# Kernel tuning notes

Measured on AMD Instinct MI355X. Metric: run time of the kernel, lower is better.

## Reference

```python
import jax, jax.numpy as jnp
import numpy as np

# Production-scale detection head dims
B_TOTAL = 16      # num_tbins(4) * batch_size(4)
NUM_ANCHORS = 100000
NUM_CLASSES = 8


def setup_inputs() -> dict:
    key = jax.random.key(0)
    k1, k2, k3, k4 = jax.random.split(key, 4)
    # anchors [A,4] = (cx, cy, w, h); widths/heights strictly positive
    ctr = jax.random.uniform(k1, (NUM_ANCHORS, 2), jnp.float32) * 512.0
    wh = jax.random.uniform(k2, (NUM_ANCHORS, 2), jnp.float32) * 64.0 + 8.0
    anchors = jnp.concatenate([ctr, wh], axis=-1)
    loc_preds = jax.random.normal(k3, (B_TOTAL, NUM_ANCHORS, 4), jnp.float32)
    # class scores in [0,1] (post-sigmoid semantics)
    cls_preds = jax.nn.sigmoid(jax.random.normal(k4, (B_TOTAL, NUM_ANCHORS, NUM_CLASSES), jnp.float32))
    return {
        "anchors": anchors,
        "loc_preds": loc_preds,
        "cls_preds": cls_preds,
        "varx": 0.1,
        "vary": 0.2,
        "score_thresh": 0.7,
        "batch_size": 4,
    }


def reference(anchors, loc_preds, cls_preds, varx, vary, score_thresh, batch_size):
    """Anchor decode + score-threshold filtering.

    Faithful to BoxDecoder.forward, but jit-compatible: instead of
    boolean-mask compaction into ragged per-(t,i) lists (data-dependent
    shapes), we return the dense [B*A*C, 6] box tensor plus the keep mask
    and batch_index; (mask, batch_index) fully determine the ragged
    targets[t][i] = box_tensor[mask & (batch_index == t*batch_size+i)].
    """
    B, A, C = cls_preds.shape
    # decode: xy = loc[:2]*varx*anchor_wh + anchor_xy ; wh = exp(loc[2:]*vary)*anchor_wh
    xy = loc_preds[..., :2] * varx * anchors[..., 2:] + anchors[..., :2]
    wh = jnp.exp(loc_preds[..., 2:] * vary) * anchors[..., 2:]
    box_preds = jnp.concatenate([xy - wh * 0.5, xy + wh * 0.5], axis=-1)  # [B,A,4]
    # expand boxes over classes, flatten to [B*A*C, ...] (same order as torch view(-1,...))
    boxes = jnp.broadcast_to(box_preds[:, :, None, :], (B, A, C, 4)).reshape(-1, 4)
    scores = cls_preds.reshape(-1)
    # idxs = b*C + c  ->  label = c+1, batch_index = b
    labels = jnp.broadcast_to(jnp.arange(C, dtype=jnp.float32) + 1.0, (B, A, C)).reshape(-1)
    batch_index = jnp.broadcast_to(jnp.arange(B, dtype=jnp.int32)[:, None, None], (B, A, C)).reshape(-1)
    box_tensor = jnp.concatenate([boxes, scores[:, None], labels[:, None]], axis=1)  # [B*A*C, 6]
    mask = scores >= score_thresh  # keep mask (compaction left to consumer / kernel)
    return box_tensor, mask, batch_index
```

## Files before the change

### kernel.cpp

```cpp
#include <hip/hip_runtime.h>
#include <math.h>


#define MAGIC_SHIFT 38

__global__ __launch_bounds__(256) void box_decode_kernel(
    const float4* __restrict__ anchors,
    const float4* __restrict__ loc,
    const float*  __restrict__ cls,
    const float*  __restrict__ varx_p,
    const float*  __restrict__ vary_p,
    const float*  __restrict__ th_p,
    float4*       __restrict__ out_box4,
    float4*       __restrict__ out_mask4,
    float4*       __restrict__ out_bidx4,
    unsigned n4,
    unsigned nm4,
    unsigned nb_box,
    unsigned A, unsigned C,
    unsigned f4_per_t,
    unsigned long long invA,
    unsigned long long invC,
    unsigned long long invF)
{
    unsigned tid = threadIdx.x;

    if (blockIdx.x < nb_box) {
        unsigned g = blockIdx.x * 256u + tid;
        if (g >= n4) return;

        unsigned t  = (unsigned)(((unsigned long long)g * invF) >> MAGIC_SHIFT);
        unsigned j  = g - t * f4_per_t;
        unsigned b  = (unsigned)(((unsigned long long)t * invA) >> MAGIC_SHIFT);
        unsigned a  = t - b * A;
        unsigned s  = j / 3u;
        unsigned jm = j - s * 3u;

        float varx = *varx_p;
        float vary = *vary_p;

        float4 anc = anchors[a];
        float4 lp  = loc[t];

        float x = fmaf(lp.x * varx, anc.z, anc.x);
        float y = fmaf(lp.y * varx, anc.w, anc.y);
        float w = expf(lp.z * vary) * anc.z;
        float h = expf(lp.w * vary) * anc.w;

        float x1 = fmaf(w, -0.5f, x);
        float y1 = fmaf(h, -0.5f, y);
        float x2 = fmaf(w,  0.5f, x);
        float y2 = fmaf(h,  0.5f, y);

        unsigned r0 = t * C + 2u * s;

        float4 r;
        if (jm == 0u) {
            r.x = x1; r.y = y1; r.z = x2; r.w = y2;
        } else if (jm == 1u) {
            r.x = cls[r0];
            r.y = (float)(2u * s + 1u);
            r.z = x1; r.w = y1;
        } else {
            r.x = x2; r.y = y2;
            r.z = cls[r0 + 1u];
            r.w = (float)(2u * s + 2u);
        }
        out_box4[g] = r;
    } else {
        unsigned k = (blockIdx.x - nb_box) * 256u + tid;
        if (k >= nm4) return;

        float th = *th_p;
        const float4* cls4 = (const float4*)cls;
        float4 sc = cls4[k];

        unsigned row0 = k * 4u;
        unsigned t2 = (unsigned)(((unsigned long long)row0 * invC) >> MAGIC_SHIFT);
        unsigned b  = (unsigned)(((unsigned long long)t2  * invA) >> MAGIC_SHIFT);
        float bf = (float)b;

        float4 m;
        m.x = (sc.x >= th) ? 1.0f : 0.0f;
        m.y = (sc.y >= th) ? 1.0f : 0.0f;
        m.z = (sc.z >= th) ? 1.0f : 0.0f;
        m.w = (sc.w >= th) ? 1.0f : 0.0f;
        out_mask4[k] = m;

        float4 bv; bv.x = bf; bv.y = bf; bv.z = bf; bv.w = bf;
        out_bidx4[k] = bv;
    }
}

extern "C" void kernel_launch(void* const* d_in, const int* in_sizes, int n_in,
                              void* d_out, int out_size, void* d_ws, size_t ws_size,
                              hipStream_t stream) {
    const float* anchors = (const float*)d_in[0];
    const float* loc     = (const float*)d_in[1];
    const float* cls     = (const float*)d_in[2];
    const float* varx_p  = (const float*)d_in[3];
    const float* vary_p  = (const float*)d_in[4];
    const float* th_p    = (const float*)d_in[5];

    unsigned A = (unsigned)(in_sizes[0] / 4);
    unsigned B = (unsigned)((unsigned)in_sizes[1] / (4u * A));
    unsigned C = (unsigned)((unsigned)in_sizes[2] / (A * B));
    unsigned rows = B * A * C;

    unsigned f4_per_t = (6u * C) / 4u;
    unsigned n4  = rows * 6u / 4u;
    unsigned nm4 = rows / 4u;

    float* out_box  = (float*)d_out;
    float* out_mask = out_box + (size_t)rows * 6;
    float* out_bidx = out_mask + rows;

    unsigned long long invA = ((1ULL << MAGIC_SHIFT) / A) + 1ULL;
    unsigned long long invC = ((1ULL << MAGIC_SHIFT) / C) + 1ULL;
    unsigned long long invF = ((1ULL << MAGIC_SHIFT) / f4_per_t) + 1ULL;

    unsigned nb_box  = (n4  + 255u) / 256u;
    unsigned nb_mask = (nm4 + 255u) / 256u;

    box_decode_kernel<<<dim3(nb_box + nb_mask), dim3(256), 0, stream>>>(
        (const float4*)anchors, (const float4*)loc, cls,
        varx_p, vary_p, th_p,
        (float4*)out_box, (float4*)out_mask, (float4*)out_bidx,
        n4, nm4, nb_box, A, C, f4_per_t, invA, invC, invF);
}
```

Before: 523.2 us.

## Fuse mask and batch-index writes into box threads with nontemporal stores

Removes the separate mask/batch-index block range. The box threads that already read each score now also write that score's mask and batch index as scalar stores, so cls is read once. All output stores become nontemporal to avoid polluting cache on this write-heavy stream. The tradeoff is that the mask and bidx writes change from float4 to scattered scalar stores, two thirds of threads now write extra, and the box threads become more divergent.

```diff
diff --git a/kernel.cpp b/kernel.cpp
--- a/kernel.cpp
+++ b/kernel.cpp
@@ -3,6 +3,8 @@
 
 
 #define MAGIC_SHIFT 38
+
+typedef float vfloat4 __attribute__((ext_vector_type(4)));
 
 __global__ __launch_bounds__(256) void box_decode_kernel(
     const float4* __restrict__ anchors,
@@ -11,85 +13,64 @@
     const float*  __restrict__ varx_p,
     const float*  __restrict__ vary_p,
     const float*  __restrict__ th_p,
-    float4*       __restrict__ out_box4,
-    float4*       __restrict__ out_mask4,
-    float4*       __restrict__ out_bidx4,
+    vfloat4*      __restrict__ out_box4,
+    float*        __restrict__ out_mask,
+    float*        __restrict__ out_bidx,
     unsigned n4,
-    unsigned nm4,
-    unsigned nb_box,
     unsigned A, unsigned C,
     unsigned f4_per_t,
     unsigned long long invA,
-    unsigned long long invC,
     unsigned long long invF)
 {
-    unsigned tid = threadIdx.x;
+    unsigned g = blockIdx.x * 256u + threadIdx.x;
+    if (g >= n4) return;
 
-    if (blockIdx.x < nb_box) {
-        unsigned g = blockIdx.x * 256u + tid;
-        if (g >= n4) return;
+    unsigned t  = (unsigned)(((unsigned long long)g * invF) >> MAGIC_SHIFT);
+    unsigned j  = g - t * f4_per_t;
+    unsigned b  = (unsigned)(((unsigned long long)t * invA) >> MAGIC_SHIFT);
+    unsigned a  = t - b * A;
+    unsigned s  = j / 3u;
+    unsigned jm = j - s * 3u;
 
-        unsigned t  = (unsigned)(((unsigned long long)g * invF) >> MAGIC_SHIFT);
-        unsigned j  = g - t * f4_per_t;
-        unsigned b  = (unsigned)(((unsigned long long)t * invA) >> MAGIC_SHIFT);
-        unsigned a  = t - b * A;
-        unsigned s  = j / 3u;
-        unsigned jm = j - s * 3u;
+    float varx = *varx_p;
+    float vary = *vary_p;
+    float th   = *th_p;
 
-        float varx = *varx_p;
-        float vary = *vary_p;
+    float4 anc = anchors[a];
+    float4 lp  = loc[t];
 
-        float4 anc = anchors[a];
-        float4 lp  = loc[t];
+    float x = fmaf(lp.x * varx, anc.z, anc.x);
+    float y = fmaf(lp.y * varx, anc.w, anc.y);
+    float w = expf(lp.z * vary) * anc.z;
+    float h = expf(lp.w * vary) * anc.w;
 
-        float x = fmaf(lp.x * varx, anc.z, anc.x);
-        float y = fmaf(lp.y * varx, anc.w, anc.y);
-        float w = expf(lp.z * vary) * anc.z;
-        float h = expf(lp.w * vary) * anc.w;
+    float x1 = fmaf(w, -0.5f, x);
+    float y1 = fmaf(h, -0.5f, y);
+    float x2 = fmaf(w,  0.5f, x);
+    float y2 = fmaf(h,  0.5f, y);
 
-        float x1 = fmaf(w, -0.5f, x);
-        float y1 = fmaf(h, -0.5f, y);
-        float x2 = fmaf(w,  0.5f, x);
-        float y2 = fmaf(h,  0.5f, y);
+    unsigned r0 = t * C + 2u * s;
+    float bf = (float)b;
 
-        unsigned r0 = t * C + 2u * s;
-
-        float4 r;
-        if (jm == 0u) {
-            r.x = x1; r.y = y1; r.z = x2; r.w = y2;
-        } else if (jm == 1u) {
-            r.x = cls[r0];
-            r.y = (float)(2u * s + 1u);
-            r.z = x1; r.w = y1;
-        } else {
-            r.x = x2; r.y = y2;
-            r.z = cls[r0 + 1u];
-            r.w = (float)(2u * s + 2u);
-        }
-        out_box4[g] = r;
+    vfloat4 r;
+    if (jm == 0u) {
+        r.x = x1; r.y = y1; r.z = x2; r.w = y2;
+    } else if (jm == 1u) {
+        float sc0 = cls[r0];
+        r.x = sc0;
+        r.y = (float)(2u * s + 1u);
+        r.z = x1; r.w = y1;
+        __builtin_nontemporal_store((sc0 >= th) ? 1.0f : 0.0f, &out_mask[r0]);
+        __builtin_nontemporal_store(bf, &out_bidx[r0]);
     } else {
-        unsigned k = (blockIdx.x - nb_box) * 256u + tid;
-        if (k >= nm4) return;
-
-        float th = *th_p;
-        const float4* cls4 = (const float4*)cls;
-        float4 sc = cls4[k];
-
-        unsigned row0 = k * 4u;
-        unsigned t2 = (unsigned)(((unsigned long long)row0 * invC) >> MAGIC_SHIFT);
-        unsigned b  = (unsigned)(((unsigned long long)t2  * invA) >> MAGIC_SHIFT);
-        float bf = (float)b;
-
-        float4 m;
-        m.x = (sc.x >= th) ? 1.0f : 0.0f;
-        m.y = (sc.y >= th) ? 1.0f : 0.0f;
-        m.z = (sc.z >= th) ? 1.0f : 0.0f;
-        m.w = (sc.w >= th) ? 1.0f : 0.0f;
-        out_mask4[k] = m;
-
-        float4 bv; bv.x = bf; bv.y = bf; bv.z = bf; bv.w = bf;
-        out_bidx4[k] = bv;
+        float sc1 = cls[r0 + 1u];
+        r.x = x2; r.y = y2;
+        r.z = sc1;
+        r.w = (float)(2u * s + 2u);
+        __builtin_nontemporal_store((sc1 >= th) ? 1.0f : 0.0f, &out_mask[r0 + 1u]);
+        __builtin_nontemporal_store(bf, &out_bidx[r0 + 1u]);
     }
+    __builtin_nontemporal_store(r, &out_box4[g]);
 }
 
 extern "C" void kernel_launch(void* const* d_in, const int* in_sizes, int n_in,
@@ -108,23 +89,19 @@
     unsigned rows = B * A * C;
 
     unsigned f4_per_t = (6u * C) / 4u;
-    unsigned n4  = rows * 6u / 4u;
-    unsigned nm4 = rows / 4u;
+    unsigned n4 = rows * 6u / 4u;
 
     float* out_box  = (float*)d_out;
     float* out_mask = out_box + (size_t)rows * 6;
     float* out_bidx = out_mask + rows;
 
     unsigned long long invA = ((1ULL << MAGIC_SHIFT) / A) + 1ULL;
-    unsigned long long invC = ((1ULL << MAGIC_SHIFT) / C) + 1ULL;
     unsigned long long invF = ((1ULL << MAGIC_SHIFT) / f4_per_t) + 1ULL;
 
-    unsigned nb_box  = (n4  + 255u) / 256u;
-    unsigned nb_mask = (nm4 + 255u) / 256u;
-
-    box_decode_kernel<<<dim3(nb_box + nb_mask), dim3(256), 0, stream>>>(
+    unsigned nb = (n4 + 255u) / 256u;
+    box_decode_kernel<<<dim3(nb), dim3(256), 0, stream>>>(
         (const float4*)anchors, (const float4*)loc, cls,
         varx_p, vary_p, th_p,
-        (float4*)out_box, (float4*)out_mask, (float4*)out_bidx,
-        n4, nm4, nb_box, A, C, f4_per_t, invA, invC, invF);
+        (vfloat4*)out_box, out_mask, out_bidx,
+        n4, A, C, f4_per_t, invA, invF);
 }
```

After: 498.6 us. -4.7%, faster.
